# Kernel optimization log

Measured on AMD Instinct MI355X. Metric: run time of the kernel, lower is better.

The kernel has to match this reference:

```python
import jax, jax.numpy as jnp
import numpy as np

N = 2048          # n_oscillators
B = 16            # batch
DT = 0.1
STEPS = 10
PHI_INV = 2.0 / (1.0 + float(np.sqrt(5.0)))  # 1/phi


def setup_inputs() -> dict:
    key = jax.random.key(0)
    k1, k2, k3 = jax.random.split(key, 3)
    theta = jax.random.normal(k1, (B, N), dtype=jnp.float32)  # phases
    K = jax.random.normal(k2, (N, N), dtype=jnp.float32) * 0.1
    K = (K + K.T) / 2  # symmetrize as in __init__
    omega = jax.random.normal(k3, (N,), dtype=jnp.float32) * 0.1
    K_global = jnp.float32(PHI_INV)
    triad_climb_mod = jnp.float32(0.2)
    return {"theta": theta, "K": K, "omega": omega,
            "K_global": K_global, "triad_climb_mod": triad_climb_mod}


def reference(theta, K, omega, K_global, triad_climb_mod):
    # Default TriadState: armed=True, unlocked=False, triad_guidance=None
    K_eff = K * (1.0 + triad_climb_mod)

    def step(th, _):
        # theta_diff[b, i, j] = th[b, j] - th[b, i]
        diff = th[..., None, :] - th[..., :, None]          # [B, N, N]
        coupling_sum = (K_eff * jnp.sin(diff)).sum(-1)      # [B, N]
        dth = omega + (K_global / N) * coupling_sum
        th = th + DT * dth
        th = jnp.arctan2(jnp.sin(th), jnp.cos(th))          # wrap to (-pi, pi]
        return th, None

    theta, _ = jax.lax.scan(step, theta, None, length=STEPS)
    coherence = jnp.sqrt(jnp.cos(theta).mean(-1) ** 2 +
                         jnp.sin(theta).mean(-1) ** 2)      # [B]
    return theta, coherence
```

## Files before the change

kernel.cpp:

```cpp
#include <hip/hip_runtime.h>
#include <math.h>

#define NOSC 2048
#define NB 16
#define DT 0.1f
#define M_TOT (NB * NOSC)
#define KTP 2056

typedef __attribute__((ext_vector_type(8))) short bf16x8;
typedef __attribute__((ext_vector_type(4))) float f32x4;

__device__ __forceinline__ unsigned short f2bf(float x) {
    unsigned int u = __float_as_uint(x);
    u += 0x7FFFu + ((u >> 16) & 1u);
    return (unsigned short)(u >> 16);
}
__device__ __forceinline__ float bf2f(unsigned short u) {
    return __uint_as_float(((unsigned int)u) << 16);
}

__device__ __forceinline__ int ridx(int c, int j) {
    return ((j >> 3) << 7) + (c << 3) + (j & 7);
}



__global__ void init_kernel(const float* __restrict__ th_in,
                            float* __restrict__ th,
                            unsigned short* __restrict__ R0) {
    const int idx = blockIdx.x * 256 + threadIdx.x;
    const int o4 = idx * 4;
    float4 v = *reinterpret_cast<const float4*>(th_in + o4);
    *reinterpret_cast<float4*>(th + o4) = v;
    const int b = o4 >> 11;
    const int j = o4 & (NOSC - 1);
    float s0, c0, s1, c1, s2, c2, s3, c3;
    sincosf(v.x, &s0, &c0); sincosf(v.y, &s1, &c1);
    sincosf(v.z, &s2, &c2); sincosf(v.w, &s3, &c3);
    const int L = ridx(b, j);
    ushort4 us = {f2bf(s0), f2bf(s1), f2bf(s2), f2bf(s3)};
    ushort4 uc = {f2bf(c0), f2bf(c1), f2bf(c2), f2bf(c3)};
    *reinterpret_cast<ushort4*>(R0 + L) = us;
    *reinterpret_cast<ushort4*>(R0 + M_TOT + L) = uc;
}

template <bool FIRST, bool FINAL>
__global__ __launch_bounds__(1024, 4) void step_kernel(
    const float* __restrict__ Kmat,
    unsigned short* __restrict__ Kbt,
    const unsigned short* __restrict__ Rc,
    unsigned short* __restrict__ Rn,
    const float* __restrict__ omega,
    const float* __restrict__ kg,
    const float* __restrict__ mod,
    float* __restrict__ th)
{
    __shared__ float part[16][2][64][4];
    __shared__ float coup[32][16];

    const int t = threadIdx.x;
    const int lane = t & 63;
    const int w = t >> 6;
    const int i0 = blockIdx.x * 16;
    const int rl = lane & 15;
    const int kbase = w * 128 + ((lane >> 4) << 3);

    float th_o = 0.0f, sin_i = 0.0f, cos_i = 0.0f, om_i = 0.0f;
    size_t o_upd = 0; int Lr = 0;
    if (t < 256) {
        const int b2 = t >> 4;
        const int il = t & 15;
        o_upd = (size_t)b2 * NOSC + i0 + il;
        Lr = ridx(b2, i0 + il);
        th_o = th[o_upd];
        sin_i = bf2f(Rc[Lr]);
        cos_i = bf2f(Rc[M_TOT + Lr]);
        om_i = omega[i0 + il];
    }
    const float scale = kg[0] * (1.0f + mod[0]) * (1.0f / (float)NOSC);

    bf16x8 as[4], ac[4], bb[4];
    unsigned short* __restrict__ kf =
        Kbt + (((size_t)blockIdx.x * 16 + w) << 11) + (lane << 3);
    if constexpr (FIRST) {
        __shared__ unsigned short Kt[16][KTP];
        const float4* __restrict__ src =
            reinterpret_cast<const float4*>(Kmat + (size_t)i0 * NOSC);
#pragma unroll
        for (int p = 0; p < 8; ++p) {
            const int q = t + p * 1024;
            float4 v = src[q];
            ushort4 u = {f2bf(v.x), f2bf(v.y), f2bf(v.z), f2bf(v.w)};
            *reinterpret_cast<ushort4*>(&Kt[q >> 9][(q & 511) * 4]) = u;
        }
        __syncthreads();
#pragma unroll
        for (int k = 0; k < 4; ++k) {
            bb[k] = *reinterpret_cast<const bf16x8*>(&Kt[rl][kbase + k * 32]);
            *reinterpret_cast<bf16x8*>(kf + (k << 9)) = bb[k];
        }
    } else {
#pragma unroll
        for (int k = 0; k < 4; ++k)
            bb[k] = *reinterpret_cast<const bf16x8*>(kf + (k << 9));
    }

    const unsigned short* __restrict__ pa = Rc + (w << 11) + (lane << 3);
#pragma unroll
    for (int k = 0; k < 4; ++k) {
        as[k] = *reinterpret_cast<const bf16x8*>(pa + (k << 9));
        ac[k] = *reinterpret_cast<const bf16x8*>(pa + M_TOT + (k << 9));
    }

    f32x4 acc_s = {0.0f, 0.0f, 0.0f, 0.0f};
    f32x4 acc_c = {0.0f, 0.0f, 0.0f, 0.0f};
#pragma unroll
    for (int k = 0; k < 4; ++k) {
        acc_s = __builtin_amdgcn_mfma_f32_16x16x32_bf16(as[k], bb[k], acc_s, 0, 0, 0);
        acc_c = __builtin_amdgcn_mfma_f32_16x16x32_bf16(ac[k], bb[k], acc_c, 0, 0, 0);
    }
    *reinterpret_cast<f32x4*>(&part[w][0][lane][0]) = acc_s;
    *reinterpret_cast<f32x4*>(&part[w][1][lane][0]) = acc_c;
    __syncthreads();

    if (t < 512) {
        const int c = t >> 4, il = t & 15;
        const int half = c >> 4, cl = c & 15;
        const int ln = ((cl >> 2) << 4) | il, rg = cl & 3;
        float s = 0.0f;
#pragma unroll
        for (int q = 0; q < 16; ++q) s += part[q][half][ln][rg];
        coup[c][il] = s;
    }
    __syncthreads();

    if (t < 256) {
        const int b2 = t >> 4;
        const int il = t & 15;
        const float aS = coup[b2][il];
        const float aC = coup[16 + b2][il];
        float nt = th_o + DT * (om_i + scale * (cos_i * aS - sin_i * aC));
        float ws, wc;
        sincosf(nt, &ws, &wc);
        th[o_upd] = FINAL ? atan2f(ws, wc) : nt;
        float sn = __shfl_down(ws, 1), cn = __shfl_down(wc, 1);
        if ((il & 1) == 0) {
            *reinterpret_cast<unsigned int*>(Rn + Lr) =
                (unsigned)f2bf(ws) | ((unsigned)f2bf(sn) << 16);
            *reinterpret_cast<unsigned int*>(Rn + M_TOT + Lr) =
                (unsigned)f2bf(wc) | ((unsigned)f2bf(cn) << 16);
        }
    }
}

__global__ void coherence_kernel(const unsigned short* __restrict__ R,
                                 float* __restrict__ coh) {
    const int b = blockIdx.x;
    const int t = threadIdx.x;
    const int j0 = t * 8;
    const int L = ridx(b, j0);
    float ss = 0.0f, sc = 0.0f;
#pragma unroll
    for (int e = 0; e < 8; ++e) {
        ss += bf2f(R[L + e]);
        sc += bf2f(R[M_TOT + L + e]);
    }
    for (int off = 32; off > 0; off >>= 1) {
        ss += __shfl_down(ss, off);
        sc += __shfl_down(sc, off);
    }
    __shared__ float red[8];
    const int w = t >> 6;
    if ((t & 63) == 0) { red[w * 2] = sc; red[w * 2 + 1] = ss; }
    __syncthreads();
    if (t == 0) {
        float tc = 0.0f, ts = 0.0f;
        for (int k = 0; k < 4; ++k) { tc += red[k * 2]; ts += red[k * 2 + 1]; }
        tc /= (float)NOSC;
        ts /= (float)NOSC;
        coh[b] = sqrtf(tc * tc + ts * ts);
    }
}

extern "C" void kernel_launch(void* const* d_in, const int* in_sizes, int n_in,
                              void* d_out, int out_size, void* d_ws, size_t ws_size,
                              hipStream_t stream) {
    const float* theta_in = (const float*)d_in[0];
    const float* Kmat     = (const float*)d_in[1];
    const float* omega    = (const float*)d_in[2];
    const float* kg       = (const float*)d_in[3];
    const float* mod      = (const float*)d_in[4];

    float* th  = (float*)d_out;
    float* coh = (float*)d_out + M_TOT;

    unsigned short* Kbt = (unsigned short*)d_ws;
    unsigned short* RA  = Kbt + (size_t)NOSC * NOSC;
    unsigned short* RB  = RA + 2 * M_TOT;

    init_kernel<<<32, 256, 0, stream>>>(theta_in, th, RA);

    for (int s = 0; s < 10; ++s) {
        const unsigned short* rc = (s & 1) ? RB : RA;
        unsigned short* rn = (s & 1) ? RA : RB;
        if (s == 0)
            step_kernel<true, false><<<NOSC / 16, 1024, 0, stream>>>(
                Kmat, Kbt, rc, rn, omega, kg, mod, th);
        else if (s < 9)
            step_kernel<false, false><<<NOSC / 16, 1024, 0, stream>>>(
                Kmat, Kbt, rc, rn, omega, kg, mod, th);
        else
            step_kernel<false, true><<<NOSC / 16, 1024, 0, stream>>>(
                Kmat, Kbt, rc, rn, omega, kg, mod, th);
    }

    coherence_kernel<<<NB, 256, 0, stream>>>(RA, coh);
}
```

Before: 57.94 us.

## Fuse init and coherence computation into step kernels to remove launches

Removes the separate init kernel by computing sin/cos of the input phases directly inside the first step kernel, both for the per-thread update values and the MFMA A fragments. Also removes the coherence kernel by reducing sin/cos sums with atomics in the final step and using a last-block ticket to compute coherence. This saves two kernel launches and their dependencies. In exchange, the first step does redundant transcendental work per block, and the final step adds atomics and a grid-wide ticket.

After: 119.6 us. 2.06x slower.

```diff
diff --git a/kernel.cpp b/kernel.cpp
--- a/kernel.cpp
+++ b/kernel.cpp
@@ -6,6 +6,7 @@
 #define DT 0.1f
 #define M_TOT (NB * NOSC)
 #define KTP 2056
+#define NBLK 128
 
 typedef __attribute__((ext_vector_type(8))) short bf16x8;
 typedef __attribute__((ext_vector_type(4))) float f32x4;
@@ -25,27 +26,9 @@
 
 
 
-__global__ void init_kernel(const float* __restrict__ th_in,
-                            float* __restrict__ th,
-                            unsigned short* __restrict__ R0) {
-    const int idx = blockIdx.x * 256 + threadIdx.x;
-    const int o4 = idx * 4;
-    float4 v = *reinterpret_cast<const float4*>(th_in + o4);
-    *reinterpret_cast<float4*>(th + o4) = v;
-    const int b = o4 >> 11;
-    const int j = o4 & (NOSC - 1);
-    float s0, c0, s1, c1, s2, c2, s3, c3;
-    sincosf(v.x, &s0, &c0); sincosf(v.y, &s1, &c1);
-    sincosf(v.z, &s2, &c2); sincosf(v.w, &s3, &c3);
-    const int L = ridx(b, j);
-    ushort4 us = {f2bf(s0), f2bf(s1), f2bf(s2), f2bf(s3)};
-    ushort4 uc = {f2bf(c0), f2bf(c1), f2bf(c2), f2bf(c3)};
-    *reinterpret_cast<ushort4*>(R0 + L) = us;
-    *reinterpret_cast<ushort4*>(R0 + M_TOT + L) = uc;
-}
-
 template <bool FIRST, bool FINAL>
 __global__ __launch_bounds__(1024, 4) void step_kernel(
+    const float* __restrict__ theta_in,
     const float* __restrict__ Kmat,
     unsigned short* __restrict__ Kbt,
     const unsigned short* __restrict__ Rc,
@@ -53,7 +36,10 @@
     const float* __restrict__ omega,
     const float* __restrict__ kg,
     const float* __restrict__ mod,
-    float* __restrict__ th)
+    float* __restrict__ th,
+    float* __restrict__ coh,
+    float* __restrict__ accum,
+    unsigned int* __restrict__ ticket)
 {
     __shared__ float part[16][2][64][4];
     __shared__ float coup[32][16];
@@ -72,17 +58,27 @@
         const int il = t & 15;
         o_upd = (size_t)b2 * NOSC + i0 + il;
         Lr = ridx(b2, i0 + il);
-        th_o = th[o_upd];
-        sin_i = bf2f(Rc[Lr]);
-        cos_i = bf2f(Rc[M_TOT + Lr]);
         om_i = omega[i0 + il];
+        if constexpr (FIRST) {
+            th_o = theta_in[o_upd];
+            sincosf(th_o, &sin_i, &cos_i);
+        } else {
+            th_o = th[o_upd];
+            sin_i = bf2f(Rc[Lr]);
+            cos_i = bf2f(Rc[M_TOT + Lr]);
+        }
     }
     const float scale = kg[0] * (1.0f + mod[0]) * (1.0f / (float)NOSC);
 
     bf16x8 as[4], ac[4], bb[4];
     unsigned short* __restrict__ kf =
         Kbt + (((size_t)blockIdx.x * 16 + w) << 11) + (lane << 3);
+
     if constexpr (FIRST) {
+        if (blockIdx.x == 0) {
+            if (t < 32) accum[t] = 0.0f;
+            if (t == 32) *ticket = 0u;
+        }
         __shared__ unsigned short Kt[16][KTP];
         const float4* __restrict__ src =
             reinterpret_cast<const float4*>(Kmat + (size_t)i0 * NOSC);
@@ -99,17 +95,30 @@
             bb[k] = *reinterpret_cast<const bf16x8*>(&Kt[rl][kbase + k * 32]);
             *reinterpret_cast<bf16x8*>(kf + (k << 9)) = bb[k];
         }
+        const float* __restrict__ tp = theta_in + (size_t)rl * NOSC + kbase;
+#pragma unroll
+        for (int k = 0; k < 4; ++k) {
+            bf16x8 a_s, a_c;
+#pragma unroll
+            for (int e = 0; e < 8; ++e) {
+                float s, c;
+                sincosf(tp[k * 32 + e], &s, &c);
+                a_s[e] = (short)f2bf(s);
+                a_c[e] = (short)f2bf(c);
+            }
+            as[k] = a_s;
+            ac[k] = a_c;
+        }
     } else {
 #pragma unroll
         for (int k = 0; k < 4; ++k)
             bb[k] = *reinterpret_cast<const bf16x8*>(kf + (k << 9));
-    }
-
-    const unsigned short* __restrict__ pa = Rc + (w << 11) + (lane << 3);
-#pragma unroll
-    for (int k = 0; k < 4; ++k) {
-        as[k] = *reinterpret_cast<const bf16x8*>(pa + (k << 9));
-        ac[k] = *reinterpret_cast<const bf16x8*>(pa + M_TOT + (k << 9));
+        const unsigned short* __restrict__ pa = Rc + (w << 11) + (lane << 3);
+#pragma unroll
+        for (int k = 0; k < 4; ++k) {
+            as[k] = *reinterpret_cast<const bf16x8*>(pa + (k << 9));
+            ac[k] = *reinterpret_cast<const bf16x8*>(pa + M_TOT + (k << 9));
+        }
     }
 
     f32x4 acc_s = {0.0f, 0.0f, 0.0f, 0.0f};
@@ -142,43 +151,42 @@
         float nt = th_o + DT * (om_i + scale * (cos_i * aS - sin_i * aC));
         float ws, wc;
         sincosf(nt, &ws, &wc);
-        th[o_upd] = FINAL ? atan2f(ws, wc) : nt;
-        float sn = __shfl_down(ws, 1), cn = __shfl_down(wc, 1);
-        if ((il & 1) == 0) {
-            *reinterpret_cast<unsigned int*>(Rn + Lr) =
-                (unsigned)f2bf(ws) | ((unsigned)f2bf(sn) << 16);
-            *reinterpret_cast<unsigned int*>(Rn + M_TOT + Lr) =
-                (unsigned)f2bf(wc) | ((unsigned)f2bf(cn) << 16);
-        }
-    }
-}
-
-__global__ void coherence_kernel(const unsigned short* __restrict__ R,
-                                 float* __restrict__ coh) {
-    const int b = blockIdx.x;
-    const int t = threadIdx.x;
-    const int j0 = t * 8;
-    const int L = ridx(b, j0);
-    float ss = 0.0f, sc = 0.0f;
-#pragma unroll
-    for (int e = 0; e < 8; ++e) {
-        ss += bf2f(R[L + e]);
-        sc += bf2f(R[M_TOT + L + e]);
-    }
-    for (int off = 32; off > 0; off >>= 1) {
-        ss += __shfl_down(ss, off);
-        sc += __shfl_down(sc, off);
-    }
-    __shared__ float red[8];
-    const int w = t >> 6;
-    if ((t & 63) == 0) { red[w * 2] = sc; red[w * 2 + 1] = ss; }
-    __syncthreads();
-    if (t == 0) {
-        float tc = 0.0f, ts = 0.0f;
-        for (int k = 0; k < 4; ++k) { tc += red[k * 2]; ts += red[k * 2 + 1]; }
-        tc /= (float)NOSC;
-        ts /= (float)NOSC;
-        coh[b] = sqrtf(tc * tc + ts * ts);
+        if constexpr (FINAL) {
+            th[o_upd] = atan2f(ws, wc);
+#pragma unroll
+            for (int m = 1; m < 16; m <<= 1) {
+                ws += __shfl_xor(ws, m);
+                wc += __shfl_xor(wc, m);
+            }
+            if (il == 0) {
+                atomicAdd(&accum[b2], ws);
+                atomicAdd(&accum[16 + b2], wc);
+            }
+        } else {
+            th[o_upd] = nt;
+            float sn = __shfl_down(ws, 1), cn = __shfl_down(wc, 1);
+            if ((il & 1) == 0) {
+                *reinterpret_cast<unsigned int*>(Rn + Lr) =
+                    (unsigned)f2bf(ws) | ((unsigned)f2bf(sn) << 16);
+                *reinterpret_cast<unsigned int*>(Rn + M_TOT + Lr) =
+                    (unsigned)f2bf(wc) | ((unsigned)f2bf(cn) << 16);
+            }
+        }
+    }
+
+    if constexpr (FINAL) {
+        __syncthreads();
+        __threadfence();
+        if (t == 0) {
+            const unsigned int tk = atomicAdd(ticket, 1u);
+            if (tk == NBLK - 1) {
+                for (int b = 0; b < NB; ++b) {
+                    float ss = atomicAdd(&accum[b], 0.0f) * (1.0f / (float)NOSC);
+                    float cc = atomicAdd(&accum[16 + b], 0.0f) * (1.0f / (float)NOSC);
+                    coh[b] = sqrtf(ss * ss + cc * cc);
+                }
+            }
+        }
     }
 }
 
@@ -197,22 +205,20 @@
     unsigned short* Kbt = (unsigned short*)d_ws;
     unsigned short* RA  = Kbt + (size_t)NOSC * NOSC;
     unsigned short* RB  = RA + 2 * M_TOT;
-
-    init_kernel<<<32, 256, 0, stream>>>(theta_in, th, RA);
+    float* accum = (float*)(RB + 2 * M_TOT);
+    unsigned int* ticket = (unsigned int*)(accum + 32);
 
     for (int s = 0; s < 10; ++s) {
         const unsigned short* rc = (s & 1) ? RB : RA;
         unsigned short* rn = (s & 1) ? RA : RB;
         if (s == 0)
-            step_kernel<true, false><<<NOSC / 16, 1024, 0, stream>>>(
-                Kmat, Kbt, rc, rn, omega, kg, mod, th);
+            step_kernel<true, false><<<NBLK, 1024, 0, stream>>>(
+                theta_in, Kmat, Kbt, rc, rn, omega, kg, mod, th, coh, accum, ticket);
         else if (s < 9)
-            step_kernel<false, false><<<NOSC / 16, 1024, 0, stream>>>(
-                Kmat, Kbt, rc, rn, omega, kg, mod, th);
+            step_kernel<false, false><<<NBLK, 1024, 0, stream>>>(
+                theta_in, Kmat, Kbt, rc, rn, omega, kg, mod, th, coh, accum, ticket);
         else
-            step_kernel<false, true><<<NOSC / 16, 1024, 0, stream>>>(
-                Kmat, Kbt, rc, rn, omega, kg, mod, th);
-    }
-
-    coherence_kernel<<<NB, 256, 0, stream>>>(RA, coh);
-}
+            step_kernel<false, true><<<NBLK, 1024, 0, stream>>>(
+                theta_in, Kmat, Kbt, rc, rn, omega, kg, mod, th, coh, accum, ticket);
+    }
+}
```
